# Kernel optimization log

Hardware: AMD Instinct MI355X
Metric: run time of the kernel (lower is better)

## Reference

```python
import jax, jax.numpy as jnp
import numpy as np

B, T, L, N = 2048, 50, 30, 1000
NF, EMB, SEMB, NWD = 2, 32, 12, 7


def setup_inputs() -> dict:
    key = jax.random.key(0)
    ks = jax.random.split(key, 12)
    return {
        "stops": jax.random.randint(ks[0], (B, T), 0, N, dtype=jnp.int32),
        "x": jax.random.normal(ks[1], (B, L, N), dtype=jnp.float32),
        "x_dist": jax.random.uniform(ks[2], (N,), dtype=jnp.float32),
        "x_features": jax.random.normal(ks[3], (B, NF), dtype=jnp.float32),
        "x_week": jax.random.randint(ks[4], (B,), 0, NWD, dtype=jnp.int32),
        "x_mask": jax.random.randint(ks[5], (B, N), 0, 2, dtype=jnp.int32),
        "emb_week": jax.random.normal(ks[6], (NWD, EMB), dtype=jnp.float32),
        "emb_stop": jax.random.normal(ks[7], (N, SEMB), dtype=jnp.float32),
        "W_l": jax.random.normal(ks[8], (1, L), dtype=jnp.float32) * 0.1,
        "b_l": jnp.zeros((1,), dtype=jnp.float32),
        "W_r": jax.random.normal(ks[9], (1, L), dtype=jnp.float32) * 0.1,
        "fc2_W": jax.random.normal(ks[10], (1, EMB + NF + 2 + SEMB), dtype=jnp.float32) * 0.1,
        "fc2_b": jnp.zeros((1,), dtype=jnp.float32),
    }


def _sage_mean_aggr(msg, dst, n_nodes):
    # msg: [E, L] source features, dst: [E] target node ids (one graph)
    s = jax.ops.segment_sum(msg, dst, num_segments=n_nodes)          # [N, L]
    c = jax.ops.segment_sum(jnp.ones(dst.shape, msg.dtype), dst, num_segments=n_nodes)
    return jnp.where(c[:, None] > 0, s / jnp.maximum(c, 1.0)[:, None], 0.0)


def reference(stops, x, x_dist, x_features, x_week, x_mask,
              emb_week, emb_stop, W_l, b_l, W_r, fc2_W, fc2_b):
    b, l, n = x.shape
    x_nodes = jnp.transpose(x, (0, 2, 1))                 # [B, N, L]  (x_train[i].t())
    # edges: (traj[i] -> traj[i+1]) within each row's graph
    src, dst = stops[:, :-1], stops[:, 1:]                # [B, T-1]
    msg = jnp.take_along_axis(x_nodes, src[:, :, None], axis=1)  # [B, E, L] gather source feats
    aggr = jax.vmap(_sage_mean_aggr, in_axes=(0, 0, None))(msg, dst, n)  # [B, N, L]
    # PyG SAGEConv: lin_l(mean-aggregated neighbors) + lin_r(root)
    out = jnp.einsum("bnl,ol->bno", aggr, W_l) + b_l + jnp.einsum("bnl,ol->bno", x_nodes, W_r)  # [B,N,1]
    # per-trajectory stop-embedding sum
    x_embed = emb_stop[stops].sum(axis=1)                 # [B, SEMB]
    x_emb = emb_week[x_week]                              # [B, EMB]
    feat = jnp.concatenate([x_emb, x_features], axis=-1)  # [B, EMB+NF]
    x_ = jnp.concatenate([
        jnp.broadcast_to(feat[:, None, :], (b, n, feat.shape[-1])),
        jnp.broadcast_to(x_embed[:, None, :], (b, n, x_embed.shape[-1])),
        out,
        jnp.broadcast_to(x_dist[None, :, None], (b, n, 1)),
    ], axis=-1)                                           # [B, N, 48]
    logits = (jnp.einsum("bnf,of->bno", x_, fc2_W) + fc2_b)[..., 0]  # [B, N]
    ls = jax.nn.log_softmax(logits, axis=1)
    return jnp.where(x_mask.astype(bool), -1e8, ls)
```

## Files before the change

kernel.cpp:

```cpp
#include <hip/hip_runtime.h>

#define Bc 2048
#define Tc 50
#define Lc 30
#define Nc 1000
#define NFc 2
#define EMBc 32
#define SEMBc 12

__global__ __launch_bounds__(256) void gnnsage_kernel(
    const int*   __restrict__ stops,
    const float* __restrict__ x,
    const float* __restrict__ x_dist,
    const float* __restrict__ x_features,
    const int*   __restrict__ x_week,
    const int*   __restrict__ x_mask,
    const float* __restrict__ emb_week,
    const float* __restrict__ emb_stop,
    const float* __restrict__ W_l,
    const float* __restrict__ b_l,
    const float* __restrict__ W_r,
    const float* __restrict__ fc2_W,
    const float* __restrict__ fc2_b,
    float*       __restrict__ out)
{
    __shared__ float sWl[Lc], sWr[Lc];
    __shared__ float wl[Nc];
    __shared__ float lg[Nc];
    __shared__ float seg_sum[Nc];
    __shared__ float seg_cnt[Nc];
    __shared__ float s_cb;
    __shared__ float s_red[4];
    __shared__ float s_bcast;

    const int b   = blockIdx.x;
    const int tid = threadIdx.x;
    const float* xb = x + (size_t)b * (Lc * Nc);
    const int*   st = stops + b * Tc;

    if (tid < Lc) { sWl[tid] = W_l[tid]; sWr[tid] = W_r[tid]; }
    for (int n = tid; n < Nc; n += 256) { seg_sum[n] = 0.f; seg_cnt[n] = 0.f; }
    if (tid == 0) {
        float cb = fc2_b[0];
        const float* ew = emb_week + x_week[b] * EMBc;
        #pragma unroll
        for (int i = 0; i < EMBc; ++i) cb += ew[i] * fc2_W[i];
        cb += x_features[b * NFc + 0] * fc2_W[EMBc + 0];
        cb += x_features[b * NFc + 1] * fc2_W[EMBc + 1];
        s_cb = cb;
    }
    __syncthreads();

    if (tid < Tc) {
        const float* es = emb_stop + st[tid] * SEMBc;
        float p = 0.f;
        #pragma unroll
        for (int i = 0; i < SEMBc; ++i) p += es[i] * fc2_W[EMBc + NFc + i];
        atomicAdd(&s_cb, p);
    }

    if (tid < Nc / 4) {
        const int n0 = tid * 4;
        float4 sl = make_float4(0.f, 0.f, 0.f, 0.f);
        float4 sr = make_float4(0.f, 0.f, 0.f, 0.f);
        #pragma unroll
        for (int l = 0; l < Lc; ++l) {
            float4 v = *reinterpret_cast<const float4*>(xb + l * Nc + n0);
            float a = sWl[l], r = sWr[l];
            sl.x += v.x * a; sl.y += v.y * a; sl.z += v.z * a; sl.w += v.w * a;
            sr.x += v.x * r; sr.y += v.y * r; sr.z += v.z * r; sr.w += v.w * r;
        }
        *reinterpret_cast<float4*>(&wl[n0]) = sl;
        *reinterpret_cast<float4*>(&lg[n0]) = sr;
    }
    __syncthreads();

    if (tid < Tc - 1) {
        int s = st[tid], d = st[tid + 1];
        atomicAdd(&seg_sum[d], wl[s]);
        atomicAdd(&seg_cnt[d], 1.0f);
    }
    __syncthreads();

    const float cb  = s_cb;
    const float w46 = fc2_W[EMBc + NFc + SEMBc];
    const float w47 = fc2_W[EMBc + NFc + SEMBc + 1];
    const float bl  = b_l[0];
    float lmax = -3.0e38f;
    for (int n = tid; n < Nc; n += 256) {
        float c = seg_cnt[n];
        float a = (c > 0.f) ? seg_sum[n] / c : 0.f;
        float v = cb + w46 * (a + bl + lg[n]) + w47 * x_dist[n];
        lg[n] = v;
        lmax = fmaxf(lmax, v);
    }

    #pragma unroll
    for (int off = 32; off > 0; off >>= 1) lmax = fmaxf(lmax, __shfl_xor(lmax, off));
    const int wid = tid >> 6;
    if ((tid & 63) == 0) s_red[wid] = lmax;
    __syncthreads();
    if (tid == 0)
        s_bcast = fmaxf(fmaxf(s_red[0], s_red[1]), fmaxf(s_red[2], s_red[3]));
    __syncthreads();
    const float mx = s_bcast;

    float lsum = 0.f;
    for (int n = tid; n < Nc; n += 256) lsum += expf(lg[n] - mx);
    #pragma unroll
    for (int off = 32; off > 0; off >>= 1) lsum += __shfl_xor(lsum, off);
    if ((tid & 63) == 0) s_red[wid] = lsum;
    __syncthreads();
    if (tid == 0) s_bcast = logf(s_red[0] + s_red[1] + s_red[2] + s_red[3]);
    __syncthreads();
    const float lse = mx + s_bcast;

    const int* mk = x_mask + (size_t)b * Nc;
    float* ob = out + (size_t)b * Nc;
    for (int n = tid; n < Nc; n += 256) {
        ob[n] = mk[n] ? -100000000.0f : (lg[n] - lse);
    }
}

extern "C" void kernel_launch(void* const* d_in, const int* in_sizes, int n_in,
                              void* d_out, int out_size, void* d_ws, size_t ws_size,
                              hipStream_t stream) {
    const int*   stops      = (const int*)  d_in[0];
    const float* x          = (const float*)d_in[1];
    const float* x_dist     = (const float*)d_in[2];
    const float* x_features = (const float*)d_in[3];
    const int*   x_week     = (const int*)  d_in[4];
    const int*   x_mask     = (const int*)  d_in[5];
    const float* emb_week   = (const float*)d_in[6];
    const float* emb_stop   = (const float*)d_in[7];
    const float* W_l        = (const float*)d_in[8];
    const float* b_l        = (const float*)d_in[9];
    const float* W_r        = (const float*)d_in[10];
    const float* fc2_W      = (const float*)d_in[11];
    const float* fc2_b      = (const float*)d_in[12];
    float* out = (float*)d_out;

    gnnsage_kernel<<<Bc, 256, 0, stream>>>(stops, x, x_dist, x_features, x_week,
                                           x_mask, emb_week, emb_stop, W_l, b_l,
                                           W_r, fc2_W, fc2_b, out);
}
```

Before: 50.28 us.

## Keep logits in registers, prefetch mask/dist, use nontemporal vector I/O

Logits now stay in per-thread float4 registers across the max, sum and output phases instead of living in a shared array, and the final pass reads and writes four values per thread. The mask and x_dist loads are issued at kernel start so their latency overlaps the main reduction over L. The stop-embedding sum moves from a shared-memory atomic to a wavefront shuffle, and neighbour stop ids come from a register shuffle. Loads of x and stores of the output use nontemporal hints and fast __expf, which adds small numerical differences.

```diff
diff --git a/kernel.cpp b/kernel.cpp
--- a/kernel.cpp
+++ b/kernel.cpp
@@ -7,6 +7,9 @@
 #define NFc 2
 #define EMBc 32
 #define SEMBc 12
+
+typedef float f4 __attribute__((ext_vector_type(4)));
+typedef int   i4 __attribute__((ext_vector_type(4)));
 
 __global__ __launch_bounds__(256) void gnnsage_kernel(
     const int*   __restrict__ stops,
@@ -26,7 +29,6 @@
 {
     __shared__ float sWl[Lc], sWr[Lc];
     __shared__ float wl[Nc];
-    __shared__ float lg[Nc];
     __shared__ float seg_sum[Nc];
     __shared__ float seg_cnt[Nc];
     __shared__ float s_cb;
@@ -36,12 +38,31 @@
     const int b   = blockIdx.x;
     const int tid = threadIdx.x;
     const float* xb = x + (size_t)b * (Lc * Nc);
-    const int*   st = stops + b * Tc;
 
     if (tid < Lc) { sWl[tid] = W_l[tid]; sWr[tid] = W_r[tid]; }
     for (int n = tid; n < Nc; n += 256) { seg_sum[n] = 0.f; seg_cnt[n] = 0.f; }
+
+    i4 mk = (i4)0;
+    f4 d4 = (f4)0.f;
+    if (tid < Nc / 4) {
+        mk = ((const i4*)(x_mask + (size_t)b * Nc))[tid];
+        d4 = ((const f4*)x_dist)[tid];
+    }
+
+    float p = 0.f;
+    int st_t = 0;
+    if (tid < Tc) {
+        st_t = stops[b * Tc + tid];
+        const float* es = emb_stop + st_t * SEMBc;
+        #pragma unroll
+        for (int i = 0; i < SEMBc; ++i) p += es[i] * fc2_W[EMBc + NFc + i];
+    }
+    if (tid < 64) {
+        #pragma unroll
+        for (int off = 32; off > 0; off >>= 1) p += __shfl_xor(p, off);
+    }
     if (tid == 0) {
-        float cb = fc2_b[0];
+        float cb = fc2_b[0] + p;
         const float* ew = emb_week + x_week[b] * EMBc;
         #pragma unroll
         for (int i = 0; i < EMBc; ++i) cb += ew[i] * fc2_W[i];
@@ -51,34 +72,25 @@
     }
     __syncthreads();
 
-    if (tid < Tc) {
-        const float* es = emb_stop + st[tid] * SEMBc;
-        float p = 0.f;
-        #pragma unroll
-        for (int i = 0; i < SEMBc; ++i) p += es[i] * fc2_W[EMBc + NFc + i];
-        atomicAdd(&s_cb, p);
-    }
-
+    f4 sr = (f4)0.f;
     if (tid < Nc / 4) {
-        const int n0 = tid * 4;
-        float4 sl = make_float4(0.f, 0.f, 0.f, 0.f);
-        float4 sr = make_float4(0.f, 0.f, 0.f, 0.f);
+        f4 sl = (f4)0.f;
         #pragma unroll
         for (int l = 0; l < Lc; ++l) {
-            float4 v = *reinterpret_cast<const float4*>(xb + l * Nc + n0);
-            float a = sWl[l], r = sWr[l];
-            sl.x += v.x * a; sl.y += v.y * a; sl.z += v.z * a; sl.w += v.w * a;
-            sr.x += v.x * r; sr.y += v.y * r; sr.z += v.z * r; sr.w += v.w * r;
+            f4 v = __builtin_nontemporal_load((const f4*)(xb + l * Nc) + tid);
+            sl += v * sWl[l];
+            sr += v * sWr[l];
         }
-        *reinterpret_cast<float4*>(&wl[n0]) = sl;
-        *reinterpret_cast<float4*>(&lg[n0]) = sr;
+        *((f4*)&wl[tid * 4]) = sl;
     }
     __syncthreads();
 
-    if (tid < Tc - 1) {
-        int s = st[tid], d = st[tid + 1];
-        atomicAdd(&seg_sum[d], wl[s]);
-        atomicAdd(&seg_cnt[d], 1.0f);
+    if (tid < 64) {
+        int d = __shfl(st_t, tid + 1);
+        if (tid < Tc - 1) {
+            atomicAdd(&seg_sum[d], wl[st_t]);
+            atomicAdd(&seg_cnt[d], 1.0f);
+        }
     }
     __syncthreads();
 
@@ -87,12 +99,18 @@
     const float w47 = fc2_W[EMBc + NFc + SEMBc + 1];
     const float bl  = b_l[0];
     float lmax = -3.0e38f;
-    for (int n = tid; n < Nc; n += 256) {
-        float c = seg_cnt[n];
-        float a = (c > 0.f) ? seg_sum[n] / c : 0.f;
-        float v = cb + w46 * (a + bl + lg[n]) + w47 * x_dist[n];
-        lg[n] = v;
-        lmax = fmaxf(lmax, v);
+    f4 v4 = (f4)0.f;
+    if (tid < Nc / 4) {
+        const int n0 = tid * 4;
+        f4 ss = *((const f4*)&seg_sum[n0]);
+        f4 sc = *((const f4*)&seg_cnt[n0]);
+        f4 a;
+        a.x = sc.x > 0.f ? ss.x / sc.x : 0.f;
+        a.y = sc.y > 0.f ? ss.y / sc.y : 0.f;
+        a.z = sc.z > 0.f ? ss.z / sc.z : 0.f;
+        a.w = sc.w > 0.f ? ss.w / sc.w : 0.f;
+        v4 = cb + w46 * (a + bl + sr) + w47 * d4;
+        lmax = fmaxf(fmaxf(v4.x, v4.y), fmaxf(v4.z, v4.w));
     }
 
     #pragma unroll
@@ -106,7 +124,8 @@
     const float mx = s_bcast;
 
     float lsum = 0.f;
-    for (int n = tid; n < Nc; n += 256) lsum += expf(lg[n] - mx);
+    if (tid < Nc / 4)
+        lsum = __expf(v4.x - mx) + __expf(v4.y - mx) + __expf(v4.z - mx) + __expf(v4.w - mx);
     #pragma unroll
     for (int off = 32; off > 0; off >>= 1) lsum += __shfl_xor(lsum, off);
     if ((tid & 63) == 0) s_red[wid] = lsum;
@@ -115,10 +134,13 @@
     __syncthreads();
     const float lse = mx + s_bcast;
 
-    const int* mk = x_mask + (size_t)b * Nc;
-    float* ob = out + (size_t)b * Nc;
-    for (int n = tid; n < Nc; n += 256) {
-        ob[n] = mk[n] ? -100000000.0f : (lg[n] - lse);
+    if (tid < Nc / 4) {
+        f4 o;
+        o.x = mk.x ? -100000000.0f : (v4.x - lse);
+        o.y = mk.y ? -100000000.0f : (v4.y - lse);
+        o.z = mk.z ? -100000000.0f : (v4.z - lse);
+        o.w = mk.w ? -100000000.0f : (v4.w - lse);
+        __builtin_nontemporal_store(o, (f4*)(out + (size_t)b * Nc) + tid);
     }
 }
 
```

Result: faster. 46.77 us (-7.0%).
